# Kernel tuning notes

Hardware: AMD Instinct MI355X
Metric: run time of the kernel (lower is better)

The kernel has to match this reference:

```python
import jax, jax.numpy as jnp
import numpy as np

B, S, H, GRID = 8, 4096, 1152, 64  # 64x64 patch grid, pooled 4x4 -> 256


def setup_inputs() -> dict:
    key = jax.random.key(0)
    k1, = jax.random.split(key, 1)
    hidden_states = jax.random.normal(k1, (B, S, H), dtype=jnp.float32)
    idx = jnp.arange(S, dtype=jnp.int32)
    pos = jnp.stack([idx % GRID, idx // GRID], axis=-1)  # (S,2) = (x,y)
    pixel_position_ids = jnp.broadcast_to(pos, (B, S, 2))
    padding_positions = jnp.zeros((B, S), dtype=bool)
    return {
        "hidden_states": hidden_states,
        "pixel_position_ids": pixel_position_ids,
        "padding_positions": padding_positions,
        "output_length": 256,
    }


def reference(hidden_states, pixel_position_ids, padding_positions, output_length):
    # 1) zero out padding rows
    hs = jnp.where(padding_positions[..., None], 0.0, hidden_states)
    hidden_size = hs.shape[-1]
    seq_len = hs.shape[1]
    k = int((seq_len // output_length) ** 0.5)
    k_sq = k * k
    assert k_sq * output_length == seq_len
    # 2) position-indexed 2D average pool via one-hot matmul
    clamped = jnp.clip(pixel_position_ids, 0).astype(jnp.int32)
    max_x = jnp.max(clamped[..., 0], axis=-1, keepdims=True) + 1  # [B,1]
    kern = clamped // k
    kernel_idxs = kern[..., 0] + (max_x // k) * kern[..., 1]  # [B,S]
    weights = jax.nn.one_hot(kernel_idxs, output_length, dtype=jnp.float32) / k_sq  # [B,S,L]
    pooled = jnp.einsum('bsl,bsh->blh', weights, hs.astype(jnp.float32)).astype(hs.dtype)
    pooler_mask = jnp.any(weights != 0, axis=1)  # [B,L]
    # 3) scale by sqrt(hidden_size)
    pooled = pooled * (hidden_size ** 0.5)
    return pooled, pooler_mask
```

## Files before the change

### kernel.cpp

```cpp
#include <hip/hip_runtime.h>
#include <math.h>

#define BB   8
#define SS   4096
#define HH   1152
#define LL   256
#define KP   4
#define KSQ  16
#define CAP  16
#define H4   (HH / 4)

__global__ __launch_bounds__(256) void build_index_kernel(
    const int* __restrict__ pos,
    int* __restrict__ counts,
    int* __restrict__ lists)
{
    const int b = blockIdx.x;
    const int t = threadIdx.x;
    const int* p = pos + (size_t)b * SS * 2;

    __shared__ int s_cnt[LL];
    __shared__ int s_wmax[4];
    __shared__ int s_stride;

    int mx = 0;
    for (int s = t; s < SS; s += 256) {
        int x = p[2 * s];
        mx = max(mx, max(x, 0));
    }
#pragma unroll
    for (int off = 32; off >= 1; off >>= 1)
        mx = max(mx, __shfl_xor(mx, off));
    if ((t & 63) == 0) s_wmax[t >> 6] = mx;

    for (int l = t; l < LL; l += 256) s_cnt[l] = 0;
    __syncthreads();

    if (t == 0) {
        int m = max(max(s_wmax[0], s_wmax[1]), max(s_wmax[2], s_wmax[3]));
        s_stride = (m + 1) / KP;
    }
    __syncthreads();
    const int stride = s_stride;

    for (int s = t; s < SS; s += 256) {
        int x = max(p[2 * s], 0);
        int y = max(p[2 * s + 1], 0);
        int kidx = x / KP + stride * (y / KP);
        if (kidx >= 0 && kidx < LL) {
            int slot = atomicAdd(&s_cnt[kidx], 1);
            if (slot < CAP)
                lists[((size_t)b * LL + kidx) * CAP + slot] = s;
        }
    }
    __syncthreads();
    for (int l = t; l < LL; l += 256) counts[b * LL + l] = s_cnt[l];
}

__global__ __launch_bounds__(256) void gather_pool_kernel(
    const float* __restrict__ hs,
    const unsigned char* __restrict__ pad,
    const int* __restrict__ counts,
    const int* __restrict__ lists,
    float* __restrict__ out)
{
    const int bl = blockIdx.x;
    const int b  = bl >> 8;
    const int t  = threadIdx.x;

    __shared__ int s_list[CAP];
    const int c  = counts[bl];
    const int cc = min(c, CAP);
    if (t < cc) s_list[t] = lists[(size_t)bl * CAP + t];
    __syncthreads();

    const float4* hb = (const float4*)hs + (size_t)b * SS * H4;
    const unsigned char* pb = pad + (size_t)b * SS;

    float4 a0 = make_float4(0.f, 0.f, 0.f, 0.f);
    float4 a1 = make_float4(0.f, 0.f, 0.f, 0.f);
    const bool has2 = t < (H4 - 256);

#pragma unroll 4
    for (int i = 0; i < cc; ++i) {
        const int s = s_list[i];
        if (pb[s]) continue;
        const float4* row = hb + (size_t)s * H4;
        float4 v0 = row[t];
        a0.x += v0.x; a0.y += v0.y; a0.z += v0.z; a0.w += v0.w;
        if (has2) {
            float4 v1 = row[t + 256];
            a1.x += v1.x; a1.y += v1.y; a1.z += v1.z; a1.w += v1.w;
        }
    }

    const float scale = sqrtf((float)HH) / (float)KSQ;
    a0.x *= scale; a0.y *= scale; a0.z *= scale; a0.w *= scale;
    a1.x *= scale; a1.y *= scale; a1.z *= scale; a1.w *= scale;

    float4* orow = (float4*)out + (size_t)bl * H4;
    orow[t] = a0;
    if (has2) orow[t + 256] = a1;

    if (t == 0)
        out[(size_t)BB * LL * HH + bl] = (c > 0) ? 1.0f : 0.0f;
}

extern "C" void kernel_launch(void* const* d_in, const int* in_sizes, int n_in,
                              void* d_out, int out_size, void* d_ws, size_t ws_size,
                              hipStream_t stream) {
    const float* hs          = (const float*)d_in[0];
    const int*   pos         = (const int*)d_in[1];
    const unsigned char* pad = (const unsigned char*)d_in[2];

    int* counts = (int*)d_ws;
    int* lists  = counts + BB * LL;

    build_index_kernel<<<BB, 256, 0, stream>>>(pos, counts, lists);
    gather_pool_kernel<<<BB * LL, 256, 0, stream>>>(hs, pad, counts, lists,
                                                    (float*)d_out);
}
```

Before: 36.42 us.

## Fuse index build into gather-pool kernel, recomputing bucket membership per block

Removes the separate index-building kernel and its global counts/lists workspace. Each output block now reads the full position array for its batch (32 KB), recomputes max_x and bucket indices, and collects its own matching tokens into shared memory before gathering rows. This saves one kernel launch and the dependency between the two kernels. In exchange, position data is read redundantly by 256 blocks per batch and each block does extra compute and a shared-memory atomic pass. The slot capacity doubles to 32 and the padding check moves into the list build.

```diff
diff --git a/kernel.cpp b/kernel.cpp
--- a/kernel.cpp
+++ b/kernel.cpp
@@ -7,89 +7,77 @@
 #define LL   256
 #define KP   4
 #define KSQ  16
-#define CAP  16
+#define CAP  32
 #define H4   (HH / 4)
+#define TPB  256
+#define TOK_PER_THR (SS / TPB)
 
-__global__ __launch_bounds__(256) void build_index_kernel(
+__global__ __launch_bounds__(TPB) void fused_pool_kernel(
+    const float* __restrict__ hs,
     const int* __restrict__ pos,
-    int* __restrict__ counts,
-    int* __restrict__ lists)
+    const unsigned char* __restrict__ pad,
+    float* __restrict__ out)
 {
-    const int b = blockIdx.x;
-    const int t = threadIdx.x;
-    const int* p = pos + (size_t)b * SS * 2;
+    const int bl = blockIdx.x;
+    const int b  = bl >> 8;
+    const int l  = bl & (LL - 1);
+    const int t  = threadIdx.x;
 
-    __shared__ int s_cnt[LL];
-    __shared__ int s_wmax[4];
-    __shared__ int s_stride;
+    const int2* p = (const int2*)(pos + (size_t)b * SS * 2);
+    const unsigned char* pb = pad + (size_t)b * SS;
 
+    int2 v[TOK_PER_THR];
     int mx = 0;
-    for (int s = t; s < SS; s += 256) {
-        int x = p[2 * s];
-        mx = max(mx, max(x, 0));
+#pragma unroll
+    for (int i = 0; i < TOK_PER_THR; ++i) {
+        v[i] = p[t + TPB * i];
+        mx = max(mx, max(v[i].x, 0));
     }
 #pragma unroll
     for (int off = 32; off >= 1; off >>= 1)
         mx = max(mx, __shfl_xor(mx, off));
+
+    __shared__ int s_wmax[TPB / 64];
+    __shared__ int s_cnt;
+    __shared__ int s_list[CAP];
+    if (t == 0) s_cnt = 0;
     if ((t & 63) == 0) s_wmax[t >> 6] = mx;
-
-    for (int l = t; l < LL; l += 256) s_cnt[l] = 0;
     __syncthreads();
 
-    if (t == 0) {
-        int m = max(max(s_wmax[0], s_wmax[1]), max(s_wmax[2], s_wmax[3]));
-        s_stride = (m + 1) / KP;
-    }
-    __syncthreads();
-    const int stride = s_stride;
+    const int m = max(max(s_wmax[0], s_wmax[1]), max(s_wmax[2], s_wmax[3]));
+    const int stride = (m + 1) / KP;
 
-    for (int s = t; s < SS; s += 256) {
-        int x = max(p[2 * s], 0);
-        int y = max(p[2 * s + 1], 0);
-        int kidx = x / KP + stride * (y / KP);
-        if (kidx >= 0 && kidx < LL) {
-            int slot = atomicAdd(&s_cnt[kidx], 1);
+#pragma unroll
+    for (int i = 0; i < TOK_PER_THR; ++i) {
+        const int x = max(v[i].x, 0);
+        const int y = max(v[i].y, 0);
+        const int kidx = x / KP + stride * (y / KP);
+        if (kidx == l) {
+            const int s = t + TPB * i;
+            const int slot = atomicAdd(&s_cnt, 1);
             if (slot < CAP)
-                lists[((size_t)b * LL + kidx) * CAP + slot] = s;
+                s_list[slot] = pb[s] ? -1 : s;
         }
     }
     __syncthreads();
-    for (int l = t; l < LL; l += 256) counts[b * LL + l] = s_cnt[l];
-}
 
-__global__ __launch_bounds__(256) void gather_pool_kernel(
-    const float* __restrict__ hs,
-    const unsigned char* __restrict__ pad,
-    const int* __restrict__ counts,
-    const int* __restrict__ lists,
-    float* __restrict__ out)
-{
-    const int bl = blockIdx.x;
-    const int b  = bl >> 8;
-    const int t  = threadIdx.x;
-
-    __shared__ int s_list[CAP];
-    const int c  = counts[bl];
+    const int c  = s_cnt;
     const int cc = min(c, CAP);
-    if (t < cc) s_list[t] = lists[(size_t)bl * CAP + t];
-    __syncthreads();
 
     const float4* hb = (const float4*)hs + (size_t)b * SS * H4;
-    const unsigned char* pb = pad + (size_t)b * SS;
 
     float4 a0 = make_float4(0.f, 0.f, 0.f, 0.f);
     float4 a1 = make_float4(0.f, 0.f, 0.f, 0.f);
-    const bool has2 = t < (H4 - 256);
+    const bool has2 = t < (H4 - TPB);
 
-#pragma unroll 4
     for (int i = 0; i < cc; ++i) {
         const int s = s_list[i];
-        if (pb[s]) continue;
+        if (s < 0) continue;
         const float4* row = hb + (size_t)s * H4;
         float4 v0 = row[t];
         a0.x += v0.x; a0.y += v0.y; a0.z += v0.z; a0.w += v0.w;
         if (has2) {
-            float4 v1 = row[t + 256];
+            float4 v1 = row[t + TPB];
             a1.x += v1.x; a1.y += v1.y; a1.z += v1.z; a1.w += v1.w;
         }
     }
@@ -100,7 +88,7 @@
 
     float4* orow = (float4*)out + (size_t)bl * H4;
     orow[t] = a0;
-    if (has2) orow[t + 256] = a1;
+    if (has2) orow[t + TPB] = a1;
 
     if (t == 0)
         out[(size_t)BB * LL * HH + bl] = (c > 0) ? 1.0f : 0.0f;
@@ -113,10 +101,5 @@
     const int*   pos         = (const int*)d_in[1];
     const unsigned char* pad = (const unsigned char*)d_in[2];
 
-    int* counts = (int*)d_ws;
-    int* lists  = counts + BB * LL;
-
-    build_index_kernel<<<BB, 256, 0, stream>>>(pos, counts, lists);
-    gather_pool_kernel<<<BB * LL, 256, 0, stream>>>(hs, pad, counts, lists,
-                                                    (float*)d_out);
+    fused_pool_kernel<<<BB * LL, TPB, 0, stream>>>(hs, pos, pad, (float*)d_out);
 }
```

Result: faster. 30.78 us (-15.5%).
